# Kernel optimization log

Measured on AMD Instinct MI355X. Metric: run time of the kernel, lower is better.

The kernel has to match this reference:

```python
import jax, jax.numpy as jnp
import numpy as np

SC = 11  # window stride / block size; unfold kernel = 3*SC = 33, padding = SC


def _unfold3(x, sc):
    """Equivalent of nn.Unfold(kernel=3*sc, stride=sc, padding=sc) on [b,c,H,W]
    where H, W are multiples of sc. Returns [b, c, 9*sc*sc, n_windows].
    Patch ordering within K differs from torch by a fixed permutation, which is
    immaterial: all contractions over K (mask, softmax, value aggregation) are
    permutation-invariant as long as the same unfold is used everywhere."""
    b, c, H, W = x.shape
    h_sc, w_sc = H // sc, W // sc
    xp = jnp.pad(x, ((0, 0), (0, 0), (sc, sc), (sc, sc)))
    blk = xp.reshape(b, c, h_sc + 2, sc, w_sc + 2, sc)
    # 3x3 neighborhood of sc-blocks around each window
    pat = jnp.stack([blk[:, :, di:di + h_sc, :, dj:dj + w_sc, :]
                     for di in range(3) for dj in range(3)], axis=2)
    # [b,c,9,h_sc,r,w_sc,s] -> [b,c,9,r,s,h_sc,w_sc] -> [b,c,9*sc*sc,n]
    pat = pat.transpose(0, 1, 2, 4, 6, 3, 5)
    return pat.reshape(b, c, 9 * sc * sc, h_sc * w_sc)


def _block_q(x, sc):
    """view(b,c,h_sc,sc,w_sc,sc).permute(0,1,2,4,3,5) -> [b,c,n,sc*sc]"""
    b, c, H, W = x.shape
    h_sc, w_sc = H // sc, W // sc
    y = x.reshape(b, c, h_sc, sc, w_sc, sc).transpose(0, 1, 2, 4, 3, 5)
    return y.reshape(b, c, h_sc * w_sc, sc * sc)


def setup_inputs() -> dict:
    key = jax.random.key(0)
    k1, k2, k3, k4, k5, k6 = jax.random.split(key, 6)
    b, c, h, w = 2, 64, 256, 256
    s = 1.0 / np.sqrt(c)
    return {
        "x_key": jax.random.normal(k1, (b, c, h, w), jnp.float32),
        "x_ref": jax.random.normal(k2, (b, c, h, w), jnp.float32),
        "Wq": jax.random.normal(k3, (c, c), jnp.float32) * s,
        "Wk": jax.random.normal(k4, (c, c), jnp.float32) * s,
        "Wv": jax.random.normal(k5, (c, c), jnp.float32) * s,
        "gamma": jax.random.normal(k6, (1,), jnp.float32) * 0.1,
    }


def reference(x_key, x_ref, Wq, Wk, Wv, gamma):
    sc = SC
    b, c, h_in, w_in = x_key.shape
    x_pad = sc - w_in % sc
    y_pad = sc - h_in % sc
    pad = ((0, 0), (0, 0), (0, y_pad), (0, x_pad))
    fk = jnp.pad(x_key, pad)
    fr = jnp.pad(x_ref, pad)
    b, c, h, w = fk.shape
    h_sc, w_sc = h // sc, w // sc

    # validity mask -> additive attention bias (out-of-image keys penalized)
    fm = jnp.pad(jnp.ones((1, 1, h_in, w_in), fk.dtype), pad)
    fm_k = _unfold3(fm, sc)          # [1,1,K,n]
    fm_q = _block_q(fm, sc)          # [1,1,n,s]
    am = (jnp.einsum('bckn,bcns->bkns', fm_k, fm_q) - 1.0) * 99.0  # [1,K,n,s]

    scale = c ** (-0.5)
    q = jnp.einsum('oi,bihw->bohw', Wq, fk)
    k = jnp.einsum('oi,bihw->bohw', Wk, fr)
    v = jnp.einsum('oi,bihw->bohw', Wv, fr)

    k_u = _unfold3(k, sc) * scale    # [b,c,K,n]
    q_b = _block_q(q, sc)            # [b,c,n,s]
    attn = jnp.einsum('bckn,bcns->bkns', k_u, q_b) + am  # [b,K,n,s]
    attn = jax.nn.softmax(attn, axis=1)

    v_u = _unfold3(v, sc)            # [b,c,K,n]
    r = jnp.einsum('bkns,bckn->bcns', attn, v_u)  # [b,c,n,s]
    r = r.reshape(b, c, h_sc, w_sc, sc, sc).transpose(0, 1, 2, 4, 3, 5)
    r = r.reshape(b, c, h, w)[:, :, :h_in, :w_in]
    return x_ref + r * gamma[0]
```

## Files before the change

### kernel.cpp

```cpp
#include <hip/hip_runtime.h>


typedef unsigned short ushort_t;
typedef unsigned int   uint32;
typedef unsigned long long uint64;
typedef __attribute__((ext_vector_type(8))) short short8;
typedef __attribute__((ext_vector_type(4))) float f32x4;

#define MFMA16(a,b,c) __builtin_amdgcn_mfma_f32_16x16x32_bf16(a,b,c,0,0,0)

#if __has_builtin(__builtin_amdgcn_exp2f)
#define EXP2(x) __builtin_amdgcn_exp2f(x)
#else
#define EXP2(x) exp2f(x)
#endif
#if __has_builtin(__builtin_amdgcn_rcpf)
#define RCP(x) __builtin_amdgcn_rcpf(x)
#else
#define RCP(x) (1.0f/(x))
#endif

#define QPKT_OFF   0u
#define KPKT_OFF   18874368u
#define VPKT_OFF   37748736u

__device__ __forceinline__ ushort_t f2bf(float f){
  union { __bf16 h; ushort_t u; } c;
  c.h = (__bf16)f;
  return c.u;
}

__device__ __forceinline__ uint32 pkbf(float a, float b){
  union { __bf16 h[2]; uint32 u; } c;
  c.h[0] = (__bf16)a;
  c.h[1] = (__bf16)b;
  return c.u;
}

__device__ __forceinline__ void storeK8(ushort_t* __restrict__ base, int nt, int t,
                                        int l15, int h, f32x4 a){
  uint32 lo = pkbf(a[0], a[1]);
  uint32 hi = pkbf(a[2], a[3]);
  int lanep = l15 + 16*((2*t + (h>>1)) & 3);
  size_t off = (size_t)((nt*2 + (t>>1))*64 + lanep)*16 + 8*(h&1);
  *(uint2*)((char*)base + off) = make_uint2(lo, hi);
}

__device__ __forceinline__ short8 ldWfrag(const float* __restrict__ W, int t, int ks,
                                          int l15, int h, float scale){
  const float* p = W + (16*t + l15)*64 + 32*ks + 8*h;
  float4 a = *(const float4*)p;
  float4 b = *(const float4*)(p + 4);
  union { uint4 u; short8 s; } x;
  x.u.x = pkbf(a.x*scale, a.y*scale);
  x.u.y = pkbf(a.z*scale, a.w*scale);
  x.u.z = pkbf(b.x*scale, b.y*scale);
  x.u.w = pkbf(b.z*scale, b.w*scale);
  return x.s;
}

__global__ __launch_bounds__(256) void proj_kernel(
    const float* __restrict__ xk, const float* __restrict__ xr,
    const float* __restrict__ Wq, const float* __restrict__ Wk, const float* __restrict__ Wv,
    ushort_t* __restrict__ qpkt, ushort_t* __restrict__ kpkt, ushort_t* __restrict__ vpkt)
{
  __shared__ __align__(16) float sX[64*192];
  const int tid = threadIdx.x;
  const int lane = tid & 63, wv = tid >> 6;
  const int l15 = lane & 15, h = lane >> 4;
  const int bid = blockIdx.x;
  const bool isQ = bid >= 1152;
  const int id = isQ ? bid - 1152 : bid;
  const int b = id / 576, rem = id % 576, ty = rem / 24, tx = rem % 24;
  const float* xs = (isQ ? xk : xr) + (size_t)b*64*65536;
  const int oy = ty*11, ox = tx*11;
  const int ox3 = ox & 3, xa = ox - ox3;

  #pragma unroll
  for (int i = tid; i < 1024; i += 256) sX[(i>>4)*192 + 176 + (i&15)] = 0.f;

  {
    const int ch = tid >> 2, seg = tid & 3;
    const float* rowp = xs + (size_t)ch*65536 + (size_t)oy*256 + (xa + 4*seg);
    float* sdst = sX + ch*192 + 4*seg;
    if (ty < 23 && tx < 23){
      #pragma unroll
      for (int y = 0; y < 11; ++y)
        *(float4*)(sdst + y*16) = *(const float4*)(rowp + y*256);
    } else {
      const int xg = xa + 4*seg;
      #pragma unroll
      for (int y = 0; y < 11; ++y){
        const bool rk = (oy + y) < 256;
        float4 v;
        v.x = (rk && xg+0 < 256) ? rowp[y*256+0] : 0.f;
        v.y = (rk && xg+1 < 256) ? rowp[y*256+1] : 0.f;
        v.z = (rk && xg+2 < 256) ? rowp[y*256+2] : 0.f;
        v.w = (rk && xg+3 < 256) ? rowp[y*256+3] : 0.f;
        *(float4*)(sdst + y*16) = v;
      }
    }
  }
  __syncthreads();

  const f32x4 zero = {0.f, 0.f, 0.f, 0.f};
  #define XFL(nt, ks, dst) { \
    const int px_ = 16*(nt) + l15; \
    const int y_ = (px_*745) >> 13; \
    const float* pp_ = sX + (32*(ks) + 8*h)*192 + y_*16 + (px_ - y_*11) + ox3; \
    union { uint4 u; short8 s; } r_; \
    r_.u.x = pkbf(pp_[0],    pp_[192]); \
    r_.u.y = pkbf(pp_[384],  pp_[576]); \
    r_.u.z = pkbf(pp_[768],  pp_[960]); \
    r_.u.w = pkbf(pp_[1152], pp_[1344]); \
    dst = r_.s; }

  if (!isQ){
    short8 wkf[4][2], wvf[4][2];
    #pragma unroll
    for (int t = 0; t < 4; ++t){
      wkf[t][0] = ldWfrag(Wk, t, 0, l15, h, 1.f);  wkf[t][1] = ldWfrag(Wk, t, 1, l15, h, 1.f);
      wvf[t][0] = ldWfrag(Wv, t, 0, l15, h, 1.f);  wvf[t][1] = ldWfrag(Wv, t, 1, l15, h, 1.f);
    }
    ushort_t* kb = kpkt + (size_t)id*8192;
    ushort_t* vb = vpkt + (size_t)id*8192;
    const int nt0 = 2*wv, nt1 = 2*wv + 1;
    short8 xf0[2], xf1[2];
    XFL(nt0, 0, xf0[0]); XFL(nt0, 1, xf0[1]);
    XFL(nt1, 0, xf1[0]); XFL(nt1, 1, xf1[1]);
    #pragma unroll
    for (int t = 0; t < 4; ++t){
      f32x4 ak0 = MFMA16(wkf[t][0], xf0[0], zero); ak0 = MFMA16(wkf[t][1], xf0[1], ak0);
      f32x4 ak1 = MFMA16(wkf[t][0], xf1[0], zero); ak1 = MFMA16(wkf[t][1], xf1[1], ak1);
      f32x4 av0 = MFMA16(xf0[0], wvf[t][0], zero); av0 = MFMA16(xf0[1], wvf[t][1], av0);
      f32x4 av1 = MFMA16(xf1[0], wvf[t][0], zero); av1 = MFMA16(xf1[1], wvf[t][1], av1);
      storeK8(kb, nt0, t, l15, h, ak0);
      storeK8(kb, nt1, t, l15, h, ak1);
      uint4 pv;
      pv.x = pkbf(av0[0], av0[1]); pv.y = pkbf(av0[2], av0[3]);
      pv.z = pkbf(av1[0], av1[1]); pv.w = pkbf(av1[2], av1[3]);
      *(uint4*)((char*)vb + (size_t)((wv*4 + t)*64 + lane)*16) = pv;
    }
  } else {
    const float C1 = 0.18033688011112042f;
    short8 wqf[4][2];
    #pragma unroll
    for (int t = 0; t < 4; ++t){
      wqf[t][0] = ldWfrag(Wq, t, 0, l15, h, C1);  wqf[t][1] = ldWfrag(Wq, t, 1, l15, h, C1);
    }
    ushort_t* qb = qpkt + (size_t)id*8192;
    #pragma unroll
    for (int nn = 0; nn < 2; ++nn){
      const int nt = 2*wv + nn;
      short8 xf[2];
      XFL(nt, 0, xf[0]); XFL(nt, 1, xf[1]);
      #pragma unroll
      for (int t = 0; t < 4; ++t){
        f32x4 aq = MFMA16(wqf[t][0], xf[0], zero); aq = MFMA16(wqf[t][1], xf[1], aq);
        storeK8(qb, nt, t, l15, h, aq);
      }
    }
  }
  #undef XFL
}

__global__ __launch_bounds__(256) void attn_kernel(
    ushort_t* qpkt,
    const ushort_t* __restrict__ kpkt, const ushort_t* __restrict__ vpkt,
    const float* __restrict__ gamma)
{
  __shared__ __align__(16) char smem[49152];
  const int tid = threadIdx.x;
  const int lane = tid & 63, wave = tid >> 6;
  const int qh = wave & 1, kh = wave >> 1;
  const int win = (blockIdx.x & 7)*144 + (blockIdx.x >> 3);
  const int b = win / 576, wid = win % 576, wy = wid / 24, wx = wid % 24;
  const int l15 = lane & 15, h = lane >> 4;

  short8 qf[4][2];
  {
    const ushort_t* qblk = qpkt + (size_t)win*8192;
    #pragma unroll
    for (int mt = 0; mt < 4; ++mt){
      qf[mt][0] = *(const short8*)(qblk + (size_t)(((4*qh+mt)*2 + 0)*64 + lane)*8);
      qf[mt][1] = *(const short8*)(qblk + (size_t)(((4*qh+mt)*2 + 1)*64 + lane)*8);
    }
  }

  uint64 cks = 0; int nv = 0;
  #pragma unroll
  for (int ck = 0; ck < 9; ++ck){
    const int ty = wy - 1 + ck/3, tx = wx - 1 + ck%3;
    if ((unsigned)ty < 24u && (unsigned)tx < 24u){
      cks |= ((uint64)ck) << (4*nv); ++nv;
    }
  }
  const int nu = 2*nv;

  const f32x4 zz = {0.f,0.f,0.f,0.f};
  f32x4 o[4][4], lsumC[4];
  #pragma unroll
  for (int mt = 0; mt < 4; ++mt){
    lsumC[mt] = zz;
    #pragma unroll
    for (int u = 0; u < 4; ++u) o[mt][u] = zz;
  }
  f32x4 init_i;
  #pragma unroll
  for (int r = 0; r < 4; ++r) init_i[r] = (4*h + r >= 9) ? -1.0e4f : 0.f;
  short8 ones;
  #pragma unroll
  for (int j = 0; j < 8; ++j) ones[j] = (short)0x3F80;

  const ushort_t* gsrc = (wave < 2) ? kpkt : vpkt;
  const int ldsoff = (wave >> 1)*8192 + (wave & 1)*4096;

  #define STAGE(u, bo) { \
    const int t_ = (u) >> 1, hf_ = (u) & 1; \
    const int ck_ = (int)((cks >> (4*t_)) & 15); \
    const int cy_ = (ck_*11) >> 5; \
    const int ty_ = wy - 1 + cy_, tx_ = wx - 1 + (ck_ - 3*cy_); \
    const char* g_ = (const char*)(gsrc + (size_t)(b*576 + ty_*24 + tx_)*8192) \
                     + hf_*8192 + (wave & 1)*4096 + lane*16; \
    char* l_ = smem + (bo)*16384 + ldsoff + lane*16; \
    _Pragma("unroll") \
    for (int i_ = 0; i_ < 4; ++i_) \
      __builtin_amdgcn_global_load_lds( \
        (const __attribute__((address_space(1))) uint32*)(g_ + i_*1024), \
        (__attribute__((address_space(3))) uint32*)(l_ + i_*1024), 16, 0, 0); \
  }

  STAGE(0, 0);
  STAGE(1, 1);

  int bu = 0;
  #pragma unroll 1
  for (int u = 0; u < nu; ++u){
    if (u + 1 < nu) { __asm__ volatile("s_waitcnt vmcnt(4)" ::: "memory"); }
    else            { __asm__ volatile("s_waitcnt vmcnt(0)" ::: "memory"); }
    __builtin_amdgcn_s_barrier();
    __asm__ volatile("" ::: "memory");

    const int bn = (bu == 2) ? 0 : bu + 1;
    const int b2 = (bn == 2) ? 0 : bn + 1;
    if (u + 2 < nu) STAGE(u + 2, b2);

    const int t = u >> 1, hf = u & 1;
    const int ckv = (int)((cks >> (4*t)) & 15);
    const int cyv = (ckv*11) >> 5;
    const int tyv = wy - 1 + cyv, txv = wx - 1 + (ckv - 3*cyv);
    const bool ey = (tyv == 23), ex = (txv == 23);
    const int ntp = 2*hf + kh;

    f32x4 b0, b1;
    if (ey | ex){
      #pragma unroll
      for (int kt = 0; kt < 2; ++kt){
        f32x4 bb;
        #pragma unroll
        for (int r = 0; r < 4; ++r){
          const int kl = 32*ntp + 16*kt + 4*h + r;
          const int ky = (kl*745) >> 13, kx = kl - ky*11;
          bool ok = (kl < 121) && (!ey || ky < 3) && (!ex || kx < 3);
          bb[r] = ok ? 0.f : -1.0e4f;
        }
        if (kt) b1 = bb; else b0 = bb;
      }
    } else {
      b0 = zz;
      b1 = (hf & kh) ? init_i : zz;
    }

    const char* lk = smem + bu*16384 + kh*4096;
    const char* lv = smem + bu*16384 + 8192 + kh*4096;
    short8 kf00 = *(const short8*)(lk + (0*64 + lane)*16);
    short8 kf01 = *(const short8*)(lk + (1*64 + lane)*16);
    short8 kf10 = *(const short8*)(lk + (2*64 + lane)*16);
    short8 kf11 = *(const short8*)(lk + (3*64 + lane)*16);
    short8 vf0  = *(const short8*)(lv + (0*64 + lane)*16);
    short8 vf1  = *(const short8*)(lv + (1*64 + lane)*16);
    short8 vf2  = *(const short8*)(lv + (2*64 + lane)*16);
    short8 vf3  = *(const short8*)(lv + (3*64 + lane)*16);

    __builtin_amdgcn_s_setprio(1);
    #pragma unroll
    for (int mt = 0; mt < 4; ++mt){
      f32x4 s0 = MFMA16(kf00, qf[mt][0], b0); s0 = MFMA16(kf01, qf[mt][1], s0);
      f32x4 s1 = MFMA16(kf10, qf[mt][0], b1); s1 = MFMA16(kf11, qf[mt][1], s1);
      float p[8];
      #pragma unroll
      for (int r = 0; r < 4; ++r){
        p[r]   = EXP2(s0[r]);
        p[4+r] = EXP2(s1[r]);
      }
      union { uint4 uu; short8 s; } af;
      af.uu.x = pkbf(p[0], p[1]); af.uu.y = pkbf(p[2], p[3]);
      af.uu.z = pkbf(p[4], p[5]); af.uu.w = pkbf(p[6], p[7]);
      o[mt][0] = MFMA16(af.s, vf0, o[mt][0]);
      o[mt][1] = MFMA16(af.s, vf1, o[mt][1]);
      o[mt][2] = MFMA16(af.s, vf2, o[mt][2]);
      o[mt][3] = MFMA16(af.s, vf3, o[mt][3]);
      lsumC[mt] = MFMA16(af.s, ones, lsumC[mt]);
    }
    __builtin_amdgcn_s_setprio(0);

    bu = bn;
  }
  #undef STAGE

  __syncthreads();
  {
    float* base = (float*)(smem + qh*12288);
    if (kh){
      #pragma unroll
      for (int mt = 0; mt < 4; ++mt){
        *(f32x4*)(base + (mt*2+0)*256 + lane*4) = o[mt][0];
        *(f32x4*)(base + (mt*2+1)*256 + lane*4) = o[mt][1];
        *(f32x4*)(base + (8+mt)*256 + lane*4)   = lsumC[mt];
      }
    }
  }
  __syncthreads();
  if (!kh){
    float* base = (float*)(smem + qh*12288);
    #pragma unroll
    for (int mt = 0; mt < 4; ++mt){
      o[mt][0] += *(const f32x4*)(base + (mt*2+0)*256 + lane*4);
      o[mt][1] += *(const f32x4*)(base + (mt*2+1)*256 + lane*4);
      lsumC[mt] += *(const f32x4*)(base + (8+mt)*256 + lane*4);
    }
  }
  __syncthreads();
  {
    float* base2 = (float*)(smem + qh*8192);
    if (kh){
      #pragma unroll
      for (int mt = 0; mt < 4; ++mt){
        *(f32x4*)(base2 + (mt*2+0)*256 + lane*4) = o[mt][2];
        *(f32x4*)(base2 + (mt*2+1)*256 + lane*4) = o[mt][3];
      }
    }
  }
  __syncthreads();
  if (!kh){
    float* base2 = (float*)(smem + qh*8192);
    #pragma unroll
    for (int mt = 0; mt < 4; ++mt){
      o[mt][2] += *(const f32x4*)(base2 + (mt*2+0)*256 + lane*4);
      o[mt][3] += *(const f32x4*)(base2 + (mt*2+1)*256 + lane*4);
    }
    const float gm = gamma[0];
    ushort_t* rb = qpkt + (size_t)win*8192 + (size_t)qh*4096;
    #pragma unroll
    for (int mt = 0; mt < 4; ++mt){
      #pragma unroll
      for (int r = 0; r < 4; ++r){
        const float wg = gm * RCP(lsumC[mt][r]);
        const int qs = 16*mt + 4*h + r;
        #pragma unroll
        for (int u = 0; u < 4; ++u)
          rb[(size_t)qs*64 + 16*u + l15] = f2bf(wg * o[mt][u][r]);
      }
    }
  }
}

__global__ __launch_bounds__(256) void ep_kernel(
    const float* __restrict__ xref, const ushort_t* __restrict__ rbuf,
    float* __restrict__ out)
{
  __shared__ float tile[64][65];
  const int tid = threadIdx.x;
  const int bidx = blockIdx.x;
  const int xc = bidx & 3, y = (bidx >> 2) & 255, b = bidx >> 10;
  const int wy = (y*745) >> 13, qy = y - wy*11;
  {
    const int ch = tid & 63, xs4 = tid >> 6;
    #pragma unroll
    for (int xi = 0; xi < 16; ++xi){
      const int xl = xi*4 + xs4;
      const int x = xc*64 + xl;
      const int wx = (x*745) >> 13, qx = x - wx*11;
      const size_t ridx = (size_t)(b*576 + wy*24 + wx)*8192 + (size_t)(qy*11 + qx)*64 + ch;
      tile[xl][ch] = __uint_as_float(((uint32)rbuf[ridx]) << 16);
    }
  }
  __syncthreads();
  {
    const int xl = tid & 63, cg = tid >> 6;
    const size_t base = (size_t)b*4194304 + (size_t)y*256 + xc*64 + xl;
    #pragma unroll
    for (int ci = 0; ci < 16; ++ci){
      const int c2 = ci*4 + cg;
      const size_t idx = base + (size_t)c2*65536;
      out[idx] = xref[idx] + tile[xl][c2];
    }
  }
}

extern "C" void kernel_launch(void* const* d_in, const int* in_sizes, int n_in,
                              void* d_out, int out_size, void* d_ws, size_t ws_size,
                              hipStream_t stream)
{
  const float* xk = (const float*)d_in[0];
  const float* xr = (const float*)d_in[1];
  const float* Wq = (const float*)d_in[2];
  const float* Wk = (const float*)d_in[3];
  const float* Wv = (const float*)d_in[4];
  const float* gm = (const float*)d_in[5];
  float* out = (float*)d_out;
  char* ws = (char*)d_ws;
  ushort_t* qp = (ushort_t*)(ws + QPKT_OFF);
  ushort_t* kp = (ushort_t*)(ws + KPKT_OFF);
  ushort_t* vp = (ushort_t*)(ws + VPKT_OFF);
  (void)in_sizes; (void)n_in; (void)out_size; (void)ws_size;

  proj_kernel<<<2304, 256, 0, stream>>>(xk, xr, Wq, Wk, Wv, qp, kp, vp);
  attn_kernel<<<1152, 256, 0, stream>>>(qp, kp, vp, gm);
  ep_kernel<<<2048, 256, 0, stream>>>(xr, qp, out);
}
```

Measured before the change: 233.0 us.

## Stage projection inputs as bf16 in LDS and vectorize epilogue loads/stores

The projection kernel now converts the input tile to bf16 once when staging into shared memory, with a padded row stride, and builds MFMA fragments from 16-bit LDS reads instead of converting floats per fragment. This halves LDS footprint and traffic. Weight fragments are loaded per output tile inside the loop rather than all held up front, which lowers register pressure. The epilogue reads two bf16 channels per 32-bit load and uses float4 loads and stores for xref and out, aiming to cut global memory transaction counts at the cost of more scattered LDS tile reads.

After: 236.7 us. Within noise of the previous version (+1.6%).

```diff
diff --git a/kernel.cpp b/kernel.cpp
--- a/kernel.cpp
+++ b/kernel.cpp
@@ -59,12 +59,13 @@
   return x.s;
 }
 
+#define SXS 196
 __global__ __launch_bounds__(256) void proj_kernel(
     const float* __restrict__ xk, const float* __restrict__ xr,
     const float* __restrict__ Wq, const float* __restrict__ Wk, const float* __restrict__ Wv,
     ushort_t* __restrict__ qpkt, ushort_t* __restrict__ kpkt, ushort_t* __restrict__ vpkt)
 {
-  __shared__ __align__(16) float sX[64*192];
+  __shared__ __align__(16) ushort_t sX[64*SXS];
   const int tid = threadIdx.x;
   const int lane = tid & 63, wv = tid >> 6;
   const int l15 = lane & 15, h = lane >> 4;
@@ -77,16 +78,18 @@
   const int ox3 = ox & 3, xa = ox - ox3;
 
   #pragma unroll
-  for (int i = tid; i < 1024; i += 256) sX[(i>>4)*192 + 176 + (i&15)] = 0.f;
+  for (int i = tid; i < 1024; i += 256) sX[(i>>4)*SXS + 176 + (i&15)] = 0;
 
   {
     const int ch = tid >> 2, seg = tid & 3;
     const float* rowp = xs + (size_t)ch*65536 + (size_t)oy*256 + (xa + 4*seg);
-    float* sdst = sX + ch*192 + 4*seg;
+    ushort_t* sdst = sX + ch*SXS + 4*seg;
     if (ty < 23 && tx < 23){
       #pragma unroll
-      for (int y = 0; y < 11; ++y)
-        *(float4*)(sdst + y*16) = *(const float4*)(rowp + y*256);
+      for (int y = 0; y < 11; ++y){
+        float4 v = *(const float4*)(rowp + y*256);
+        *(uint2*)(sdst + y*16) = make_uint2(pkbf(v.x, v.y), pkbf(v.z, v.w));
+      }
     } else {
       const int xg = xa + 4*seg;
       #pragma unroll
@@ -97,7 +100,7 @@
         v.y = (rk && xg+1 < 256) ? rowp[y*256+1] : 0.f;
         v.z = (rk && xg+2 < 256) ? rowp[y*256+2] : 0.f;
         v.w = (rk && xg+3 < 256) ? rowp[y*256+3] : 0.f;
-        *(float4*)(sdst + y*16) = v;
+        *(uint2*)(sdst + y*16) = make_uint2(pkbf(v.x, v.y), pkbf(v.z, v.w));
       }
     }
   }
@@ -107,21 +110,15 @@
   #define XFL(nt, ks, dst) { \
     const int px_ = 16*(nt) + l15; \
     const int y_ = (px_*745) >> 13; \
-    const float* pp_ = sX + (32*(ks) + 8*h)*192 + y_*16 + (px_ - y_*11) + ox3; \
+    const ushort_t* pp_ = sX + (32*(ks) + 8*h)*SXS + y_*16 + (px_ - y_*11) + ox3; \
     union { uint4 u; short8 s; } r_; \
-    r_.u.x = pkbf(pp_[0],    pp_[192]); \
-    r_.u.y = pkbf(pp_[384],  pp_[576]); \
-    r_.u.z = pkbf(pp_[768],  pp_[960]); \
-    r_.u.w = pkbf(pp_[1152], pp_[1344]); \
+    r_.u.x = (uint32)pp_[0*SXS] | ((uint32)pp_[1*SXS] << 16); \
+    r_.u.y = (uint32)pp_[2*SXS] | ((uint32)pp_[3*SXS] << 16); \
+    r_.u.z = (uint32)pp_[4*SXS] | ((uint32)pp_[5*SXS] << 16); \
+    r_.u.w = (uint32)pp_[6*SXS] | ((uint32)pp_[7*SXS] << 16); \
     dst = r_.s; }
 
   if (!isQ){
-    short8 wkf[4][2], wvf[4][2];
-    #pragma unroll
-    for (int t = 0; t < 4; ++t){
-      wkf[t][0] = ldWfrag(Wk, t, 0, l15, h, 1.f);  wkf[t][1] = ldWfrag(Wk, t, 1, l15, h, 1.f);
-      wvf[t][0] = ldWfrag(Wv, t, 0, l15, h, 1.f);  wvf[t][1] = ldWfrag(Wv, t, 1, l15, h, 1.f);
-    }
     ushort_t* kb = kpkt + (size_t)id*8192;
     ushort_t* vb = vpkt + (size_t)id*8192;
     const int nt0 = 2*wv, nt1 = 2*wv + 1;
@@ -130,10 +127,12 @@
     XFL(nt1, 0, xf1[0]); XFL(nt1, 1, xf1[1]);
     #pragma unroll
     for (int t = 0; t < 4; ++t){
-      f32x4 ak0 = MFMA16(wkf[t][0], xf0[0], zero); ak0 = MFMA16(wkf[t][1], xf0[1], ak0);
-      f32x4 ak1 = MFMA16(wkf[t][0], xf1[0], zero); ak1 = MFMA16(wkf[t][1], xf1[1], ak1);
-      f32x4 av0 = MFMA16(xf0[0], wvf[t][0], zero); av0 = MFMA16(xf0[1], wvf[t][1], av0);
-      f32x4 av1 = MFMA16(xf1[0], wvf[t][0], zero); av1 = MFMA16(xf1[1], wvf[t][1], av1);
+      short8 wk0 = ldWfrag(Wk, t, 0, l15, h, 1.f), wk1 = ldWfrag(Wk, t, 1, l15, h, 1.f);
+      short8 wv0 = ldWfrag(Wv, t, 0, l15, h, 1.f), wv1 = ldWfrag(Wv, t, 1, l15, h, 1.f);
+      f32x4 ak0 = MFMA16(wk0, xf0[0], zero); ak0 = MFMA16(wk1, xf0[1], ak0);
+      f32x4 ak1 = MFMA16(wk0, xf1[0], zero); ak1 = MFMA16(wk1, xf1[1], ak1);
+      f32x4 av0 = MFMA16(xf0[0], wv0, zero); av0 = MFMA16(xf0[1], wv1, av0);
+      f32x4 av1 = MFMA16(xf1[0], wv0, zero); av1 = MFMA16(xf1[1], wv1, av1);
       storeK8(kb, nt0, t, l15, h, ak0);
       storeK8(kb, nt1, t, l15, h, ak1);
       uint4 pv;
@@ -143,26 +142,23 @@
     }
   } else {
     const float C1 = 0.18033688011112042f;
-    short8 wqf[4][2];
+    ushort_t* qb = qpkt + (size_t)id*8192;
+    short8 xf[2][2];
+    XFL(2*wv + 0, 0, xf[0][0]); XFL(2*wv + 0, 1, xf[0][1]);
+    XFL(2*wv + 1, 0, xf[1][0]); XFL(2*wv + 1, 1, xf[1][1]);
     #pragma unroll
     for (int t = 0; t < 4; ++t){
-      wqf[t][0] = ldWfrag(Wq, t, 0, l15, h, C1);  wqf[t][1] = ldWfrag(Wq, t, 1, l15, h, C1);
-    }
-    ushort_t* qb = qpkt + (size_t)id*8192;
-    #pragma unroll
-    for (int nn = 0; nn < 2; ++nn){
-      const int nt = 2*wv + nn;
-      short8 xf[2];
-      XFL(nt, 0, xf[0]); XFL(nt, 1, xf[1]);
-      #pragma unroll
-      for (int t = 0; t < 4; ++t){
-        f32x4 aq = MFMA16(wqf[t][0], xf[0], zero); aq = MFMA16(wqf[t][1], xf[1], aq);
-        storeK8(qb, nt, t, l15, h, aq);
+      short8 wq0 = ldWfrag(Wq, t, 0, l15, h, C1), wq1 = ldWfrag(Wq, t, 1, l15, h, C1);
+      #pragma unroll
+      for (int nn = 0; nn < 2; ++nn){
+        f32x4 aq = MFMA16(wq0, xf[nn][0], zero); aq = MFMA16(wq1, xf[nn][1], aq);
+        storeK8(qb, 2*wv + nn, t, l15, h, aq);
       }
     }
   }
   #undef XFL
 }
+#undef SXS
 
 __global__ __launch_bounds__(256) void attn_kernel(
     ushort_t* qpkt,
@@ -375,25 +371,35 @@
   const int xc = bidx & 3, y = (bidx >> 2) & 255, b = bidx >> 10;
   const int wy = (y*745) >> 13, qy = y - wy*11;
   {
-    const int ch = tid & 63, xs4 = tid >> 6;
-    #pragma unroll
-    for (int xi = 0; xi < 16; ++xi){
-      const int xl = xi*4 + xs4;
+    const int ch2 = tid & 31;
+    const int xg  = tid >> 5;
+    #pragma unroll
+    for (int xi = 0; xi < 8; ++xi){
+      const int xl = xi*8 + xg;
       const int x = xc*64 + xl;
       const int wx = (x*745) >> 13, qx = x - wx*11;
-      const size_t ridx = (size_t)(b*576 + wy*24 + wx)*8192 + (size_t)(qy*11 + qx)*64 + ch;
-      tile[xl][ch] = __uint_as_float(((uint32)rbuf[ridx]) << 16);
-    }
-  }
-  __syncthreads();
-  {
-    const int xl = tid & 63, cg = tid >> 6;
-    const size_t base = (size_t)b*4194304 + (size_t)y*256 + xc*64 + xl;
-    #pragma unroll
-    for (int ci = 0; ci < 16; ++ci){
-      const int c2 = ci*4 + cg;
+      const size_t ridx = (size_t)(b*576 + wy*24 + wx)*8192 + (size_t)(qy*11 + qx)*64;
+      const uint32 v = *(const uint32*)(rbuf + ridx + 2*ch2);
+      tile[xl][2*ch2]     = __uint_as_float(v << 16);
+      tile[xl][2*ch2 + 1] = __uint_as_float(v & 0xFFFF0000u);
+    }
+  }
+  __syncthreads();
+  {
+    const int lr = tid & 15;
+    const int cg = tid >> 4;
+    const size_t base = (size_t)b*4194304 + (size_t)y*256 + xc*64 + 4*lr;
+    #pragma unroll
+    for (int ci = 0; ci < 4; ++ci){
+      const int c2 = cg + 16*ci;
       const size_t idx = base + (size_t)c2*65536;
-      out[idx] = xref[idx] + tile[xl][c2];
+      float4 xv = *(const float4*)(xref + idx);
+      float4 ov;
+      ov.x = xv.x + tile[4*lr + 0][c2];
+      ov.y = xv.y + tile[4*lr + 1][c2];
+      ov.z = xv.z + tile[4*lr + 2][c2];
+      ov.w = xv.w + tile[4*lr + 3][c2];
+      *(float4*)(out + idx) = ov;
     }
   }
 }
```
